# Optimization experiments

Hardware: AMD Instinct MI355X
Metric: run time of the kernel (lower is better)

## Reference

```python
import jax, jax.numpy as jnp
import numpy as np

B, I, H, V = 256, 512, 1024, 512


def _lstm_cell(x, h, c, W, U, b):
    # Keras LSTMCell: z = x@kernel + h@recurrent_kernel + bias, gate order i,f,g,o
    z = x @ W + h @ U + b  # [B, 4H]
    i, f, g, o = jnp.split(z, 4, axis=-1)
    i = jax.nn.sigmoid(i)
    f = jax.nn.sigmoid(f)
    g = jnp.tanh(g)
    o = jax.nn.sigmoid(o)
    c_new = f * c + i * g
    h_new = o * jnp.tanh(c_new)
    return h_new, c_new


def setup_inputs() -> dict:
    key = jax.random.key(0)
    ks = jax.random.split(key, 16)
    s_in = 1.0 / np.sqrt(I)
    s_h = 1.0 / np.sqrt(H)
    inp = {
        'x': jax.random.normal(ks[0], (B, I), jnp.float32),
        'h0': jax.random.normal(ks[1], (B, H), jnp.float32) * 0.1,
        'c0': jax.random.normal(ks[2], (B, H), jnp.float32) * 0.1,
        'h1': jax.random.normal(ks[3], (B, H), jnp.float32) * 0.1,
        'c1': jax.random.normal(ks[4], (B, H), jnp.float32) * 0.1,
        'h2': jax.random.normal(ks[5], (B, H), jnp.float32) * 0.1,
        'c2': jax.random.normal(ks[6], (B, H), jnp.float32) * 0.1,
        'W0': jax.random.normal(ks[7], (I, 4 * H), jnp.float32) * s_in,
        'U0': jax.random.normal(ks[8], (H, 4 * H), jnp.float32) * s_h,
        'b0': jnp.zeros((4 * H,), jnp.float32),
        'W1': jax.random.normal(ks[9], (H, 4 * H), jnp.float32) * s_h,
        'U1': jax.random.normal(ks[10], (H, 4 * H), jnp.float32) * s_h,
        'b1': jnp.zeros((4 * H,), jnp.float32),
        'W2': jax.random.normal(ks[11], (H, 4 * H), jnp.float32) * s_h,
        'U2': jax.random.normal(ks[12], (H, 4 * H), jnp.float32) * s_h,
        'b2': jnp.zeros((4 * H,), jnp.float32),
        'Wp': jax.random.normal(ks[13], (H, V), jnp.float32) * s_h,
        'bp': jnp.zeros((V,), jnp.float32),
    }
    return inp


def reference(x, h0, c0, h1, c1, h2, c2, W0, U0, b0, W1, U1, b1, W2, U2, b2, Wp, bp):
    # Stacked LSTM cells: output of each cell feeds the next
    h0n, c0n = _lstm_cell(x, h0, c0, W0, U0, b0)
    h1n, c1n = _lstm_cell(h0n, h1, c1, W1, U1, b1)
    h2n, c2n = _lstm_cell(h1n, h2, c2, W2, U2, b2)
    # Dense output projection on final cell output
    step_logits = h2n @ Wp + bp  # [B, V]
    return (step_logits, h0n, c0n, h1n, c1n, h2n, c2n)
```

## Files before the change

kernel.cpp:

```cpp
#include <hip/hip_runtime.h>


typedef __attribute__((ext_vector_type(8))) short short8_t;
typedef __attribute__((ext_vector_type(8))) unsigned short ushort8_t;
typedef __attribute__((ext_vector_type(4))) unsigned short ushort4_t;
typedef __attribute__((ext_vector_type(4))) float f32x4;

__device__ __forceinline__ unsigned short f2bf(float f) {
    union { float f; unsigned u; } v; v.f = f;
    unsigned r = v.u + 0x7FFFu + ((v.u >> 16) & 1u);
    return (unsigned short)(r >> 16);
}

#define KT 64
#define BN 32
#define SLOT 1048576

__global__ __launch_bounds__(512, 4)
void gemm32(const unsigned short* __restrict__ A1, const float* __restrict__ W1, int K1,
            const unsigned short* __restrict__ A2, const float* __restrict__ W2,
            int N, int Ktot, int lgs, float* __restrict__ zp)
{
    __shared__ unsigned short Al0[256 * KT];
    __shared__ unsigned short Al1[256 * KT];
    __shared__ unsigned short Wl0[BN * KT];
    __shared__ unsigned short Wl1[BN * KT];

    const int tid  = threadIdx.x;
    const int lane = tid & 63;
    const int w    = tid >> 6;
    const int lg   = lane >> 4;
    const int lr   = lane & 15;
    const int nsplit = 1 << lgs;
    const int kb   = blockIdx.x & (nsplit - 1);
    const int ns   = blockIdx.x >> lgs;
    const int n0   = ns * BN;
    const int m0   = w * 32;
    const int klen = Ktot >> lgs;
    const int kbeg = kb * klen;
    const int nt   = klen >> 6;

    const int wkr = tid >> 3;
    const int wcq = tid & 7;

    ushort8_t paA[4], paB[4];
    f32x4     pwA = {0,0,0,0}, pwB = {0,0,0,0};

    f32x4 acc00 = {0,0,0,0}, acc01 = {0,0,0,0}, acc10 = {0,0,0,0}, acc11 = {0,0,0,0};

    auto issue = [&](int t, ushort8_t (&pa)[4], f32x4& pw) {
        int k0 = kbeg + t * KT;
        const unsigned short* A; const float* Wm; int ldA, krel;
        if (k0 < K1) { A = A1; Wm = W1; ldA = K1;        krel = k0; }
        else         { A = A2; Wm = W2; ldA = Ktot - K1; krel = k0 - K1; }
#pragma unroll
        for (int it = 0; it < 4; ++it) {
            int c = tid + it * 512;
            int row = c >> 3, cc = c & 7;
            pa[it] = *(const ushort8_t*)(A + (size_t)row * ldA + krel + cc * 8);
        }
        pw = *(const f32x4*)(Wm + (size_t)(krel + wkr) * N + n0 + wcq * 4);
    };

    auto stage = [&](ushort8_t (&pa)[4], f32x4& pw,
                     unsigned short* al, unsigned short* wl) {
#pragma unroll
        for (int it = 0; it < 4; ++it) {
            int c = tid + it * 512;
            int row = c >> 3, cc = c & 7;
            *(ushort8_t*)(al + row * KT + ((cc ^ (row & 7)) << 3)) = pa[it];
        }
        unsigned short bs[4] = { f2bf(pw[0]), f2bf(pw[1]), f2bf(pw[2]), f2bf(pw[3]) };
        int kch = wkr >> 3, kwi = wkr & 7;
#pragma unroll
        for (int j = 0; j < 4; ++j) {
            int n = wcq * 4 + j;
            wl[n * KT + ((kch ^ (n & 7)) << 3) + kwi] = bs[j];
        }
    };

    auto compute = [&](const unsigned short* al, const unsigned short* wl) {
#pragma unroll
        for (int ks = 0; ks < 2; ++ks) {
            int ch = ks * 4 + lg;
            int nb0 = lr, nb1 = 16 + lr;
            short8_t b0f = *(const short8_t*)(wl + nb0 * KT + ((ch ^ (nb0 & 7)) << 3));
            short8_t b1f = *(const short8_t*)(wl + nb1 * KT + ((ch ^ (nb1 & 7)) << 3));
            int r0 = m0 + lr, r1 = m0 + 16 + lr;
            short8_t a0f = *(const short8_t*)(al + r0 * KT + ((ch ^ (r0 & 7)) << 3));
            short8_t a1f = *(const short8_t*)(al + r1 * KT + ((ch ^ (r1 & 7)) << 3));
            acc00 = __builtin_amdgcn_mfma_f32_16x16x32_bf16(a0f, b0f, acc00, 0, 0, 0);
            acc01 = __builtin_amdgcn_mfma_f32_16x16x32_bf16(a0f, b1f, acc01, 0, 0, 0);
            acc10 = __builtin_amdgcn_mfma_f32_16x16x32_bf16(a1f, b0f, acc10, 0, 0, 0);
            acc11 = __builtin_amdgcn_mfma_f32_16x16x32_bf16(a1f, b1f, acc11, 0, 0, 0);
        }
    };

#define BAR() do { asm volatile("s_waitcnt lgkmcnt(0)" ::: "memory"); \
                   __builtin_amdgcn_s_barrier(); } while (0)

    issue(0, paA, pwA);
    stage(paA, pwA, Al0, Wl0);
    if (1 < nt) issue(1, paB, pwB);
    BAR();

    for (int t = 0; t < nt; t += 2) {
        if (t + 2 < nt) issue(t + 2, paA, pwA);
        if (t + 1 < nt) stage(paB, pwB, Al1, Wl1);
        compute(Al0, Wl0);
        BAR();
        if (t + 1 < nt) {
            if (t + 3 < nt) issue(t + 3, paB, pwB);
            if (t + 2 < nt) stage(paA, pwA, Al0, Wl0);
            compute(Al1, Wl1);
            BAR();
        }
    }
#undef BAR

    float* zrow = zp + (size_t)kb * 256 * N;
#pragma unroll
    for (int r = 0; r < 4; ++r) {
        int ma = m0 + lg * 4 + r;
        int mb = ma + 16;
        zrow[(size_t)ma * N + n0 + lr]      = acc00[r];
        zrow[(size_t)ma * N + n0 + 16 + lr] = acc01[r];
        zrow[(size_t)mb * N + n0 + lr]      = acc10[r];
        zrow[(size_t)mb * N + n0 + 16 + lr] = acc11[r];
    }
}

__global__ __launch_bounds__(256)
void lstm_gates(const float* __restrict__ zp, int nsplit,
                const float* __restrict__ bias, const float* __restrict__ c_old,
                float* __restrict__ h_out, float* __restrict__ c_out,
                unsigned short* __restrict__ h_bf)
{
    int t = blockIdx.x * 256 + threadIdx.x;
    int b = t >> 8;
    int n = (t & 255) << 2;
    f32x4 iv = *(const f32x4*)(bias + n);
    f32x4 fv = *(const f32x4*)(bias + 1024 + n);
    f32x4 gv = *(const f32x4*)(bias + 2048 + n);
    f32x4 ov = *(const f32x4*)(bias + 3072 + n);
    for (int kb = 0; kb < nsplit; ++kb) {
        const float* z = zp + (size_t)kb * SLOT + (size_t)b * 4096;
        iv += *(const f32x4*)(z + n);
        fv += *(const f32x4*)(z + 1024 + n);
        gv += *(const f32x4*)(z + 2048 + n);
        ov += *(const f32x4*)(z + 3072 + n);
    }
    f32x4 cv = *(const f32x4*)(c_old + (size_t)b * 1024 + n);

    f32x4 hn, cn;
    ushort4_t hb;
#pragma unroll
    for (int j = 0; j < 4; ++j) {
        float ii = 1.f / (1.f + __expf(-iv[j]));
        float ff = 1.f / (1.f + __expf(-fv[j]));
        float gg = tanhf(gv[j]);
        float oo = 1.f / (1.f + __expf(-ov[j]));
        float c2 = ff * cv[j] + ii * gg;
        cn[j] = c2;
        float h2 = oo * tanhf(c2);
        hn[j] = h2;
        hb[j] = f2bf(h2);
    }
    *(f32x4*)(c_out + (size_t)b * 1024 + n) = cn;
    *(f32x4*)(h_out + (size_t)b * 1024 + n) = hn;
    *(ushort4_t*)(h_bf + (size_t)b * 1024 + n) = hb;
}

__global__ __launch_bounds__(256)
void finalize_proj(const float* __restrict__ zp, int nsplit,
                   const float* __restrict__ bp, float* __restrict__ logits)
{
    int t = blockIdx.x * 256 + threadIdx.x;
    int i = t * 4;
    f32x4 v = *(const f32x4*)(bp + (i & 511));
    for (int kb = 0; kb < nsplit; ++kb)
        v += *(const f32x4*)(zp + (size_t)kb * 131072 + i);
    *(f32x4*)(logits + i) = v;
}

__global__ __launch_bounds__(256)
void pack_bf16(const float* __restrict__ x,  const float* __restrict__ h0,
               const float* __restrict__ h1, const float* __restrict__ h2,
               unsigned short* __restrict__ xb,  unsigned short* __restrict__ h0b,
               unsigned short* __restrict__ h1b, unsigned short* __restrict__ h2b)
{
    int t = blockIdx.x * 256 + threadIdx.x;
    const float* src; unsigned short* dst; int off;
    if (t < 32768)       { src = x;  dst = xb;  off = t; }
    else if (t < 98304)  { src = h0; dst = h0b; off = t - 32768; }
    else if (t < 163840) { src = h1; dst = h1b; off = t - 98304; }
    else                 { src = h2; dst = h2b; off = t - 163840; }
    f32x4 v = *(const f32x4*)(src + (size_t)off * 4);
    ushort4_t o;
#pragma unroll
    for (int j = 0; j < 4; ++j) o[j] = f2bf(v[j]);
    *(ushort4_t*)(dst + (size_t)off * 4) = o;
}

extern "C" void kernel_launch(void* const* d_in, const int* in_sizes, int n_in,
                              void* d_out, int out_size, void* d_ws, size_t ws_size,
                              hipStream_t stream)
{
    const float* x  = (const float*)d_in[0];
    const float* h0 = (const float*)d_in[1];
    const float* c0 = (const float*)d_in[2];
    const float* h1 = (const float*)d_in[3];
    const float* c1 = (const float*)d_in[4];
    const float* h2 = (const float*)d_in[5];
    const float* c2 = (const float*)d_in[6];
    const float* W0 = (const float*)d_in[7];
    const float* U0 = (const float*)d_in[8];
    const float* b0 = (const float*)d_in[9];
    const float* W1 = (const float*)d_in[10];
    const float* U1 = (const float*)d_in[11];
    const float* b1 = (const float*)d_in[12];
    const float* W2 = (const float*)d_in[13];
    const float* U2 = (const float*)d_in[14];
    const float* b2 = (const float*)d_in[15];
    const float* Wp = (const float*)d_in[16];
    const float* bp = (const float*)d_in[17];

    float* out    = (float*)d_out;
    float* logits = out;
    float* h0n = out + 131072;
    float* c0n = h0n + 262144;
    float* h1n = c0n + 262144;
    float* c1n = h1n + 262144;
    float* h2n = c1n + 262144;
    float* c2n = h2n + 262144;

    const size_t need4 = 16777216ull + 262144ull + 6ull * 524288ull;
    const size_t need2 = 8388608ull  + 262144ull + 6ull * 524288ull;
    const int lgs    = (ws_size >= need4) ? 2 : (ws_size >= need2) ? 1 : 0;
    const int nsplit = 1 << lgs;
    const size_t zbytes = (size_t)nsplit * 4194304ull;

    char* ws = (char*)d_ws;
    float*          zp   = (float*)ws;
    unsigned short* xb   = (unsigned short*)(ws + zbytes);
    unsigned short* h0b  = (unsigned short*)(ws + zbytes + 262144);
    unsigned short* h1b  = (unsigned short*)(ws + zbytes + 262144 + 524288);
    unsigned short* h2b  = (unsigned short*)(ws + zbytes + 262144 + 2*524288);
    unsigned short* h0nb = (unsigned short*)(ws + zbytes + 262144 + 3*524288);
    unsigned short* h1nb = (unsigned short*)(ws + zbytes + 262144 + 4*524288);
    unsigned short* h2nb = (unsigned short*)(ws + zbytes + 262144 + 5*524288);

    pack_bf16<<<896, 256, 0, stream>>>(x, h0, h1, h2, xb, h0b, h1b, h2b);

    gemm32<<<128 * nsplit, 512, 0, stream>>>(xb, W0, 512, h0b, U0, 4096, 1536, lgs, zp);
    lstm_gates<<<256, 256, 0, stream>>>(zp, nsplit, b0, c0, h0n, c0n, h0nb);

    gemm32<<<128 * nsplit, 512, 0, stream>>>(h0nb, W1, 1024, h1b, U1, 4096, 2048, lgs, zp);
    lstm_gates<<<256, 256, 0, stream>>>(zp, nsplit, b1, c1, h1n, c1n, h1nb);

    gemm32<<<128 * nsplit, 512, 0, stream>>>(h1nb, W2, 1024, h2b, U2, 4096, 2048, lgs, zp);
    lstm_gates<<<256, 256, 0, stream>>>(zp, nsplit, b2, c2, h2n, c2n, h2nb);

    gemm32<<<16 * 8, 512, 0, stream>>>(h2nb, Wp, 1024,
                                       (const unsigned short*)nullptr,
                                       (const float*)nullptr, 512, 1024, 3, zp);
    finalize_proj<<<128, 256, 0, stream>>>(zp, 8, bp, logits);
}
```

Before: 77.57 us.

## Widen GEMM N-tile to 128 with 4x4 MFMA per wave and deeper split-K

Replaces the 32-column GEMM tile with a 128-column tile in which each wave computes a 64x64 sub-block using 4x4 MFMA accumulators. This raises arithmetic intensity and reuse of A fragments from LDS. Weight loads are reorganised so each thread converts 8 k-values to one vectorised LDS store. To keep the grid filled, split-K rises to 8 for the LSTM layers and 16 for the projection, which adds partial-sum traffic and reduction work in the gate and finalize kernels. It also raises register pressure, and launch bounds now allow only 2 blocks per unit.

```diff
diff --git a/kernel.cpp b/kernel.cpp
--- a/kernel.cpp
+++ b/kernel.cpp
@@ -5,6 +5,7 @@
 typedef __attribute__((ext_vector_type(8))) unsigned short ushort8_t;
 typedef __attribute__((ext_vector_type(4))) unsigned short ushort4_t;
 typedef __attribute__((ext_vector_type(4))) float f32x4;
+typedef __attribute__((ext_vector_type(2))) float f32x2;
 
 __device__ __forceinline__ unsigned short f2bf(float f) {
     union { float f; unsigned u; } v; v.f = f;
@@ -13,42 +14,45 @@
 }
 
 #define KT 64
-#define BN 32
+#define BN 128
 #define SLOT 1048576
 
-__global__ __launch_bounds__(512, 4)
-void gemm32(const unsigned short* __restrict__ A1, const float* __restrict__ W1, int K1,
-            const unsigned short* __restrict__ A2, const float* __restrict__ W2,
-            int N, int Ktot, int lgs, float* __restrict__ zp)
-{
-    __shared__ unsigned short Al0[256 * KT];
-    __shared__ unsigned short Al1[256 * KT];
-    __shared__ unsigned short Wl0[BN * KT];
-    __shared__ unsigned short Wl1[BN * KT];
+__global__ __launch_bounds__(512, 2)
+void gemm128(const unsigned short* __restrict__ A1, const float* __restrict__ W1, int K1,
+             const unsigned short* __restrict__ A2, const float* __restrict__ W2,
+             int N, int Ktot, int lgs, float* __restrict__ zp)
+{
+    __shared__ unsigned short Al[2][256 * KT];
+    __shared__ unsigned short Wl[2][BN * KT];
 
     const int tid  = threadIdx.x;
     const int lane = tid & 63;
     const int w    = tid >> 6;
+    const int mg   = w >> 1;
+    const int ng   = w & 1;
     const int lg   = lane >> 4;
     const int lr   = lane & 15;
     const int nsplit = 1 << lgs;
     const int kb   = blockIdx.x & (nsplit - 1);
     const int ns   = blockIdx.x >> lgs;
     const int n0   = ns * BN;
-    const int m0   = w * 32;
     const int klen = Ktot >> lgs;
     const int kbeg = kb * klen;
     const int nt   = klen >> 6;
 
-    const int wkr = tid >> 3;
-    const int wcq = tid & 7;
+    const int wnp  = tid >> 3;
+    const int woct = tid & 7;
 
     ushort8_t paA[4], paB[4];
-    f32x4     pwA = {0,0,0,0}, pwB = {0,0,0,0};
-
-    f32x4 acc00 = {0,0,0,0}, acc01 = {0,0,0,0}, acc10 = {0,0,0,0}, acc11 = {0,0,0,0};
-
-    auto issue = [&](int t, ushort8_t (&pa)[4], f32x4& pw) {
+    f32x2     pwA[8], pwB[8];
+
+    f32x4 acc[4][4];
+#pragma unroll
+    for (int i = 0; i < 4; ++i)
+#pragma unroll
+        for (int j = 0; j < 4; ++j) acc[i][j] = f32x4{0.f, 0.f, 0.f, 0.f};
+
+    auto issue = [&](int t, ushort8_t (&pa)[4], f32x2 (&pw)[8]) {
         int k0 = kbeg + t * KT;
         const unsigned short* A; const float* Wm; int ldA, krel;
         if (k0 < K1) { A = A1; Wm = W1; ldA = K1;        krel = k0; }
@@ -59,10 +63,13 @@
             int row = c >> 3, cc = c & 7;
             pa[it] = *(const ushort8_t*)(A + (size_t)row * ldA + krel + cc * 8);
         }
-        pw = *(const f32x4*)(Wm + (size_t)(krel + wkr) * N + n0 + wcq * 4);
+        const float* wb = Wm + (size_t)(krel + woct * 8) * N + n0 + wnp * 2;
+#pragma unroll
+        for (int k = 0; k < 8; ++k)
+            pw[k] = *(const f32x2*)(wb + (size_t)k * N);
     };
 
-    auto stage = [&](ushort8_t (&pa)[4], f32x4& pw,
+    auto stage = [&](ushort8_t (&pa)[4], f32x2 (&pw)[8],
                      unsigned short* al, unsigned short* wl) {
 #pragma unroll
         for (int it = 0; it < 4; ++it) {
@@ -70,12 +77,13 @@
             int row = c >> 3, cc = c & 7;
             *(ushort8_t*)(al + row * KT + ((cc ^ (row & 7)) << 3)) = pa[it];
         }
-        unsigned short bs[4] = { f2bf(pw[0]), f2bf(pw[1]), f2bf(pw[2]), f2bf(pw[3]) };
-        int kch = wkr >> 3, kwi = wkr & 7;
-#pragma unroll
-        for (int j = 0; j < 4; ++j) {
-            int n = wcq * 4 + j;
-            wl[n * KT + ((kch ^ (n & 7)) << 3) + kwi] = bs[j];
+#pragma unroll
+        for (int c = 0; c < 2; ++c) {
+            int n = wnp * 2 + c;
+            ushort8_t v;
+#pragma unroll
+            for (int k = 0; k < 8; ++k) v[k] = f2bf(pw[k][c]);
+            *(ushort8_t*)(wl + n * KT + ((woct ^ (n & 7)) << 3)) = v;
         }
     };
 
@@ -83,16 +91,23 @@
 #pragma unroll
         for (int ks = 0; ks < 2; ++ks) {
             int ch = ks * 4 + lg;
-            int nb0 = lr, nb1 = 16 + lr;
-            short8_t b0f = *(const short8_t*)(wl + nb0 * KT + ((ch ^ (nb0 & 7)) << 3));
-            short8_t b1f = *(const short8_t*)(wl + nb1 * KT + ((ch ^ (nb1 & 7)) << 3));
-            int r0 = m0 + lr, r1 = m0 + 16 + lr;
-            short8_t a0f = *(const short8_t*)(al + r0 * KT + ((ch ^ (r0 & 7)) << 3));
-            short8_t a1f = *(const short8_t*)(al + r1 * KT + ((ch ^ (r1 & 7)) << 3));
-            acc00 = __builtin_amdgcn_mfma_f32_16x16x32_bf16(a0f, b0f, acc00, 0, 0, 0);
-            acc01 = __builtin_amdgcn_mfma_f32_16x16x32_bf16(a0f, b1f, acc01, 0, 0, 0);
-            acc10 = __builtin_amdgcn_mfma_f32_16x16x32_bf16(a1f, b0f, acc10, 0, 0, 0);
-            acc11 = __builtin_amdgcn_mfma_f32_16x16x32_bf16(a1f, b1f, acc11, 0, 0, 0);
+            short8_t af[4], bf[4];
+#pragma unroll
+            for (int mi = 0; mi < 4; ++mi) {
+                int r = mg * 64 + mi * 16 + lr;
+                af[mi] = *(const short8_t*)(al + r * KT + ((ch ^ (r & 7)) << 3));
+            }
+#pragma unroll
+            for (int ni = 0; ni < 4; ++ni) {
+                int n = ng * 64 + ni * 16 + lr;
+                bf[ni] = *(const short8_t*)(wl + n * KT + ((ch ^ (n & 7)) << 3));
+            }
+#pragma unroll
+            for (int mi = 0; mi < 4; ++mi)
+#pragma unroll
+                for (int ni = 0; ni < 4; ++ni)
+                    acc[mi][ni] = __builtin_amdgcn_mfma_f32_16x16x32_bf16(
+                        af[mi], bf[ni], acc[mi][ni], 0, 0, 0);
         }
     };
 
@@ -100,19 +115,19 @@
                    __builtin_amdgcn_s_barrier(); } while (0)
 
     issue(0, paA, pwA);
-    stage(paA, pwA, Al0, Wl0);
+    stage(paA, pwA, Al[0], Wl[0]);
     if (1 < nt) issue(1, paB, pwB);
     BAR();
 
     for (int t = 0; t < nt; t += 2) {
         if (t + 2 < nt) issue(t + 2, paA, pwA);
-        if (t + 1 < nt) stage(paB, pwB, Al1, Wl1);
-        compute(Al0, Wl0);
+        if (t + 1 < nt) stage(paB, pwB, Al[1], Wl[1]);
+        compute(Al[0], Wl[0]);
         BAR();
         if (t + 1 < nt) {
             if (t + 3 < nt) issue(t + 3, paB, pwB);
-            if (t + 2 < nt) stage(paA, pwA, Al0, Wl0);
-            compute(Al1, Wl1);
+            if (t + 2 < nt) stage(paA, pwA, Al[0], Wl[0]);
+            compute(Al[1], Wl[1]);
             BAR();
         }
     }
@@ -120,14 +135,15 @@
 
     float* zrow = zp + (size_t)kb * 256 * N;
 #pragma unroll
-    for (int r = 0; r < 4; ++r) {
-        int ma = m0 + lg * 4 + r;
-        int mb = ma + 16;
-        zrow[(size_t)ma * N + n0 + lr]      = acc00[r];
-        zrow[(size_t)ma * N + n0 + 16 + lr] = acc01[r];
-        zrow[(size_t)mb * N + n0 + lr]      = acc10[r];
-        zrow[(size_t)mb * N + n0 + 16 + lr] = acc11[r];
-    }
+    for (int mi = 0; mi < 4; ++mi)
+#pragma unroll
+        for (int ni = 0; ni < 4; ++ni)
+#pragma unroll
+            for (int r = 0; r < 4; ++r) {
+                int row = mg * 64 + mi * 16 + lg * 4 + r;
+                int col = n0 + ng * 64 + ni * 16 + lr;
+                zrow[(size_t)row * N + col] = acc[mi][ni][r];
+            }
 }
 
 __global__ __launch_bounds__(256)
@@ -234,9 +250,11 @@
     float* h2n = c1n + 262144;
     float* c2n = h2n + 262144;
 
-    const size_t need4 = 16777216ull + 262144ull + 6ull * 524288ull;
-    const size_t need2 = 8388608ull  + 262144ull + 6ull * 524288ull;
-    const int lgs    = (ws_size >= need4) ? 2 : (ws_size >= need2) ? 1 : 0;
+    const size_t bfB = 262144ull + 6ull * 524288ull;
+    int lgs;
+    if      (ws_size >= 8 * 4194304ull + bfB) lgs = 3;
+    else if (ws_size >= 4 * 4194304ull + bfB) lgs = 2;
+    else                                      lgs = 1;
     const int nsplit = 1 << lgs;
     const size_t zbytes = (size_t)nsplit * 4194304ull;
 
@@ -252,17 +270,17 @@
 
     pack_bf16<<<896, 256, 0, stream>>>(x, h0, h1, h2, xb, h0b, h1b, h2b);
 
-    gemm32<<<128 * nsplit, 512, 0, stream>>>(xb, W0, 512, h0b, U0, 4096, 1536, lgs, zp);
+    gemm128<<<32 * nsplit, 512, 0, stream>>>(xb, W0, 512, h0b, U0, 4096, 1536, lgs, zp);
     lstm_gates<<<256, 256, 0, stream>>>(zp, nsplit, b0, c0, h0n, c0n, h0nb);
 
-    gemm32<<<128 * nsplit, 512, 0, stream>>>(h0nb, W1, 1024, h1b, U1, 4096, 2048, lgs, zp);
+    gemm128<<<32 * nsplit, 512, 0, stream>>>(h0nb, W1, 1024, h1b, U1, 4096, 2048, lgs, zp);
     lstm_gates<<<256, 256, 0, stream>>>(zp, nsplit, b1, c1, h1n, c1n, h1nb);
 
-    gemm32<<<128 * nsplit, 512, 0, stream>>>(h1nb, W2, 1024, h2b, U2, 4096, 2048, lgs, zp);
+    gemm128<<<32 * nsplit, 512, 0, stream>>>(h1nb, W2, 1024, h2b, U2, 4096, 2048, lgs, zp);
     lstm_gates<<<256, 256, 0, stream>>>(zp, nsplit, b2, c2, h2n, c2n, h2nb);
 
-    gemm32<<<16 * 8, 512, 0, stream>>>(h2nb, Wp, 1024,
-                                       (const unsigned short*)nullptr,
-                                       (const float*)nullptr, 512, 1024, 3, zp);
-    finalize_proj<<<128, 256, 0, stream>>>(zp, 8, bp, logits);
-}
+    gemm128<<<4 * 16, 512, 0, stream>>>(h2nb, Wp, 1024,
+                                        (const unsigned short*)nullptr,
+                                        (const float*)nullptr, 512, 1024, 4, zp);
+    finalize_proj<<<128, 256, 0, stream>>>(zp, 16, bp, logits);
+}
```

Result: slower. 98.14 us (+26.5%).
